# Kernel tuning notes

Hardware: AMD Instinct MI355X
Metric: run time of the kernel (lower is better)

Reference implementation:

```python
import jax, jax.numpy as jnp
import numpy as np

N_NODES = 100000  # number of graph nodes (adj is [N,N])


def setup_inputs() -> dict:
    key = jax.random.key(0)
    k1, k2, k3, k4 = jax.random.split(key, 4)
    E = 3200000
    D = 16
    row = jnp.sort(jax.random.randint(k1, (E,), 0, N_NODES, dtype=jnp.int32))
    col = jax.random.randint(k2, (E,), 0, N_NODES, dtype=jnp.int32)
    vals = jax.random.uniform(k3, (E,), dtype=jnp.float32)
    embeds = jax.random.normal(k4, (N_NODES, D), dtype=jnp.float32)
    return {"row": row, "col": col, "vals": vals, "embeds": embeds}


def reference(row, col, vals, embeds):
    # out = A @ embeds, A given in COO form: A[row[e], col[e]] = vals[e]
    # gather source features, scale by edge weight, scatter-add into rows
    msgs = vals[:, None] * embeds[col]  # [E, D]
    out = jax.ops.segment_sum(msgs, row, num_segments=N_NODES)  # [N, D]
    return out
```

## Files before the change

kernel.cpp:

```cpp
#include <hip/hip_runtime.h>
#include <hip/hip_fp16.h>


#define D 16
constexpr int BLOCK = 256;
constexpr int NPB = 64;
constexpr int SMEM_E = 3072;

typedef float f32x4 __attribute__((ext_vector_type(4)));
typedef int   i32x4 __attribute__((ext_vector_type(4)));
typedef unsigned int u32x2 __attribute__((ext_vector_type(2)));
typedef unsigned int u32x4 __attribute__((ext_vector_type(4)));

__device__ __forceinline__ unsigned cvIdx(unsigned i) { return i + ((i >> 6) << 2); }

__device__ __forceinline__ float2 h2f(unsigned u) {
  union { unsigned u; __half2 h; } c; c.u = u;
  return __half22float2(c.h);
}

__global__ __launch_bounds__(BLOCK) void prep_kernel(
    const int* __restrict__ row, int E,
    const float* __restrict__ embeds, int N,
    int* __restrict__ row_ptr, __half* __restrict__ table) {
  const long long t = (long long)blockIdx.x * BLOCK + threadIdx.x;

  if (table != nullptr) {
    if (t < (long long)N * 2) {
      const f32x4* src = (const f32x4*)embeds + t * 2;
      f32x4 a = src[0];
      f32x4 b = src[1];
      union { __half2 h[4]; u32x4 u; } o;
      o.h[0] = __floats2half2_rn(a[0], a[1]);
      o.h[1] = __floats2half2_rn(a[2], a[3]);
      o.h[2] = __floats2half2_rn(b[0], b[1]);
      o.h[3] = __floats2half2_rn(b[2], b[3]);
      *((u32x4*)table + t) = o.u;
    }
  }

  const long long e = t * 4;
  if (e < E) {
    int prev = (e == 0) ? -1 : row[e - 1];
    const int cnt = (E - e >= 4) ? 4 : (int)(E - e);
    int r[4];
    if (cnt == 4) {
      i32x4 r4 = *(const i32x4*)(row + e);
      r[0] = r4[0]; r[1] = r4[1]; r[2] = r4[2]; r[3] = r4[3];
    } else {
      for (int k = 0; k < cnt; ++k) r[k] = row[e + k];
    }
    for (int k = 0; k < cnt; ++k) {
      for (int n = prev + 1; n <= r[k]; ++n) row_ptr[n] = (int)e + k;
      prev = r[k];
    }
    if (e + cnt == E) {
      for (int n = prev + 1; n <= N; ++n) row_ptr[n] = E;
    }
  }
}

__device__ __forceinline__ void ldmeta(const unsigned* __restrict__ s_cv,
                                       unsigned i0, u32x4 M[4]) {
  const unsigned ci = cvIdx(i0 * 2);
  M[0] = *(const u32x4*)(s_cv + ci);
  M[1] = *(const u32x4*)(s_cv + ci + 4);
  M[2] = *(const u32x4*)(s_cv + ci + 8);
  M[3] = *(const u32x4*)(s_cv + ci + 12);
}

__device__ __forceinline__ void gath(const char* __restrict__ tb,
                                     const u32x4 M[4], unsigned q8, u32x2 G[8]) {
  G[0] = *(const u32x2*)(tb + (size_t)(M[0][0] << 5) + q8);
  G[1] = *(const u32x2*)(tb + (size_t)(M[0][2] << 5) + q8);
  G[2] = *(const u32x2*)(tb + (size_t)(M[1][0] << 5) + q8);
  G[3] = *(const u32x2*)(tb + (size_t)(M[1][2] << 5) + q8);
  G[4] = *(const u32x2*)(tb + (size_t)(M[2][0] << 5) + q8);
  G[5] = *(const u32x2*)(tb + (size_t)(M[2][2] << 5) + q8);
  G[6] = *(const u32x2*)(tb + (size_t)(M[3][0] << 5) + q8);
  G[7] = *(const u32x2*)(tb + (size_t)(M[3][2] << 5) + q8);
}

__device__ __forceinline__ void cons8(f32x4& acc, const u32x4 M[4],
                                      const u32x2 G[8], int e, int gb,
                                      unsigned span) {
  const unsigned vv[8] = {M[0][1], M[0][3], M[1][1], M[1][3],
                          M[2][1], M[2][3], M[3][1], M[3][3]};
  #pragma unroll
  for (int i = 0; i < 8; ++i) {
    const float w = ((unsigned)(e + i - gb) < span) ? __uint_as_float(vv[i]) : 0.f;
    const float2 lo = h2f(G[i][0]), hi = h2f(G[i][1]);
    acc[0] = fmaf(w, lo.x, acc[0]);
    acc[1] = fmaf(w, lo.y, acc[1]);
    acc[2] = fmaf(w, hi.x, acc[2]);
    acc[3] = fmaf(w, hi.y, acc[3]);
  }
}

__global__ __launch_bounds__(BLOCK) void gcn_half_kernel(
    const int* __restrict__ col, const float* __restrict__ vals,
    const __half* __restrict__ table, const int* __restrict__ row_ptr,
    f32x4* __restrict__ out4, int N, int E) {
  __shared__ __align__(16) unsigned s_cv[SMEM_E * 2 + (SMEM_E * 2 / 64) * 4];

  const int t = threadIdx.x;
  const int n0 = blockIdx.x * NPB;
  const int nEnd = (n0 + NPB < N) ? n0 + NPB : N;
  const int g = t >> 2;
  const unsigned q8 = (unsigned)((t & 3) << 3);
  const int node = n0 + g;
  const bool active = (node < nEnd);

  const int Wb = row_ptr[n0] & ~3;
  const int We = row_ptr[nEnd];
  const int beg = active ? row_ptr[node] : 0;
  const int end = active ? row_ptr[node + 1] : 0;
  const char* tb = (const char*)table;

  f32x4 acc = {0.f, 0.f, 0.f, 0.f};

  for (int W0 = Wb; W0 < We; W0 += SMEM_E) {
    const int cnt  = (SMEM_E < We - W0) ? SMEM_E : (We - W0);
    const int cntP = (cnt + 7) & ~7;
    __syncthreads();
    for (int i = t * 4; i < cntP; i += BLOCK * 4) {
      const int e = W0 + i;
      unsigned c[4], v[4];
      if (e + 3 < E) {
        i32x4 c4 = *(const i32x4*)(col + e);
        f32x4 v4 = *(const f32x4*)(vals + e);
        #pragma unroll
        for (int k = 0; k < 4; ++k) {
          c[k] = (unsigned)c4[k];
          v[k] = __float_as_uint(v4[k]);
        }
      } else {
        #pragma unroll
        for (int k = 0; k < 4; ++k) {
          const bool ok = (e + k < E);
          c[k] = ok ? (unsigned)col[e + k] : 0u;
          v[k] = ok ? __float_as_uint(vals[e + k]) : 0u;
        }
      }
      *(u32x4*)(s_cv + cvIdx((unsigned)i * 2))     = (u32x4){c[0], v[0], c[1], v[1]};
      *(u32x4*)(s_cv + cvIdx((unsigned)i * 2) + 4) = (u32x4){c[2], v[2], c[3], v[3]};
    }
    __syncthreads();

    const int gb = (beg > W0) ? beg : W0;
    const int ge = (end < W0 + cnt) ? end : (W0 + cnt);
    if (ge > gb) {
      const unsigned span = (unsigned)(ge - gb);
      const int e0 = W0 + ((gb - W0) & ~7);
      const int e1 = e0 + ((ge - e0 + 7) & ~7);
      const int eL = e1 - 8;

      u32x4 M0[4], M1[4], M2[4];
      u32x2 G0[8], G1[8];
      const int p1 = (e0 + 8 < eL) ? e0 + 8 : eL;
      ldmeta(s_cv, (unsigned)(e0 - W0), M0);
      ldmeta(s_cv, (unsigned)(p1 - W0), M1);
      gath(tb, M0, q8, G0);

      for (int e = e0; e < e1; e += 8) {
        const int p2 = (e + 16 < eL) ? e + 16 : eL;
        ldmeta(s_cv, (unsigned)(p2 - W0), M2);
        gath(tb, M1, q8, G1);
        __builtin_amdgcn_sched_barrier(0);
        cons8(acc, M0, G0, e, gb, span);
        #pragma unroll
        for (int j = 0; j < 4; ++j) { M0[j] = M1[j]; M1[j] = M2[j]; }
        #pragma unroll
        for (int j = 0; j < 8; ++j) { G0[j] = G1[j]; }
      }
    }
  }

  if (active) {
    __builtin_nontemporal_store(acc, out4 + (size_t)node * 4 + (t & 3));
  }
}

__global__ __launch_bounds__(BLOCK) void gcn_node_f32_kernel(
    const int* __restrict__ col, const float* __restrict__ vals,
    const f32x4* __restrict__ embeds4, const int* __restrict__ row_ptr,
    f32x4* __restrict__ out4, int N, int E) {
  const int t = blockIdx.x * BLOCK + threadIdx.x;
  const int node = t >> 2;
  const int q = t & 3;
  if (node >= N) return;
  const int beg = row_ptr[node];
  const int end = row_ptr[node + 1];
  f32x4 acc = {0.f, 0.f, 0.f, 0.f};
  for (int e = beg; e < end; ++e) {
    acc += vals[e] * embeds4[(long long)col[e] * 4 + q];
  }
  __builtin_nontemporal_store(acc, out4 + (long long)node * 4 + q);
}

extern "C" void kernel_launch(void* const* d_in, const int* in_sizes, int n_in,
                              void* d_out, int out_size, void* d_ws, size_t ws_size,
                              hipStream_t stream) {
  const int*   row    = (const int*)d_in[0];
  const int*   col    = (const int*)d_in[1];
  const float* vals   = (const float*)d_in[2];
  const float* embeds = (const float*)d_in[3];

  const int E = in_sizes[0];
  const int N = in_sizes[3] / D;

  const size_t rp_bytes  = ((size_t)(N + 1) * 4 + 511) & ~(size_t)511;
  const size_t tbl_bytes = (size_t)N * D * sizeof(__half);
  const bool use_half = (ws_size >= rp_bytes + tbl_bytes) && (E >= 8);

  int*    row_ptr = (int*)d_ws;
  __half* table   = use_half ? (__half*)((char*)d_ws + rp_bytes) : nullptr;

  {
    long long chunksB = ((long long)E + 3) / 4;
    long long chunksA = use_half ? (long long)N * 2 : 0;
    long long threads = chunksB > chunksA ? chunksB : chunksA;
    int grid = (int)((threads + BLOCK - 1) / BLOCK);
    prep_kernel<<<grid, BLOCK, 0, stream>>>(row, E, embeds, N, row_ptr, table);
  }
  if (use_half) {
    const int grid = (N + NPB - 1) / NPB;
    gcn_half_kernel<<<grid, BLOCK, 0, stream>>>(
        col, vals, table, row_ptr, (f32x4*)d_out, N, E);
  } else {
    long long threads = (long long)N * 4;
    int grid = (int)((threads + BLOCK - 1) / BLOCK);
    gcn_node_f32_kernel<<<grid, BLOCK, 0, stream>>>(
        col, vals, (const f32x4*)embeds, row_ptr, (f32x4*)d_out, N, E);
  }
}
```

Before: 40.58 us.

## Split edges across lane pairs with 16-byte gathers and shuffle reduction

```diff
diff --git a/kernel.cpp b/kernel.cpp
--- a/kernel.cpp
+++ b/kernel.cpp
@@ -9,7 +9,6 @@
 
 typedef float f32x4 __attribute__((ext_vector_type(4)));
 typedef int   i32x4 __attribute__((ext_vector_type(4)));
-typedef unsigned int u32x2 __attribute__((ext_vector_type(2)));
 typedef unsigned int u32x4 __attribute__((ext_vector_type(4)));
 
 __device__ __forceinline__ unsigned cvIdx(unsigned i) { return i + ((i >> 6) << 2); }
@@ -60,54 +59,19 @@
   }
 }
 
-__device__ __forceinline__ void ldmeta(const unsigned* __restrict__ s_cv,
-                                       unsigned i0, u32x4 M[4]) {
-  const unsigned ci = cvIdx(i0 * 2);
-  M[0] = *(const u32x4*)(s_cv + ci);
-  M[1] = *(const u32x4*)(s_cv + ci + 4);
-  M[2] = *(const u32x4*)(s_cv + ci + 8);
-  M[3] = *(const u32x4*)(s_cv + ci + 12);
-}
-
-__device__ __forceinline__ void gath(const char* __restrict__ tb,
-                                     const u32x4 M[4], unsigned q8, u32x2 G[8]) {
-  G[0] = *(const u32x2*)(tb + (size_t)(M[0][0] << 5) + q8);
-  G[1] = *(const u32x2*)(tb + (size_t)(M[0][2] << 5) + q8);
-  G[2] = *(const u32x2*)(tb + (size_t)(M[1][0] << 5) + q8);
-  G[3] = *(const u32x2*)(tb + (size_t)(M[1][2] << 5) + q8);
-  G[4] = *(const u32x2*)(tb + (size_t)(M[2][0] << 5) + q8);
-  G[5] = *(const u32x2*)(tb + (size_t)(M[2][2] << 5) + q8);
-  G[6] = *(const u32x2*)(tb + (size_t)(M[3][0] << 5) + q8);
-  G[7] = *(const u32x2*)(tb + (size_t)(M[3][2] << 5) + q8);
-}
-
-__device__ __forceinline__ void cons8(f32x4& acc, const u32x4 M[4],
-                                      const u32x2 G[8], int e, int gb,
-                                      unsigned span) {
-  const unsigned vv[8] = {M[0][1], M[0][3], M[1][1], M[1][3],
-                          M[2][1], M[2][3], M[3][1], M[3][3]};
-  #pragma unroll
-  for (int i = 0; i < 8; ++i) {
-    const float w = ((unsigned)(e + i - gb) < span) ? __uint_as_float(vv[i]) : 0.f;
-    const float2 lo = h2f(G[i][0]), hi = h2f(G[i][1]);
-    acc[0] = fmaf(w, lo.x, acc[0]);
-    acc[1] = fmaf(w, lo.y, acc[1]);
-    acc[2] = fmaf(w, hi.x, acc[2]);
-    acc[3] = fmaf(w, hi.y, acc[3]);
-  }
-}
-
 __global__ __launch_bounds__(BLOCK) void gcn_half_kernel(
     const int* __restrict__ col, const float* __restrict__ vals,
     const __half* __restrict__ table, const int* __restrict__ row_ptr,
-    f32x4* __restrict__ out4, int N, int E) {
+    float* __restrict__ out, int N, int E) {
   __shared__ __align__(16) unsigned s_cv[SMEM_E * 2 + (SMEM_E * 2 / 64) * 4];
 
   const int t = threadIdx.x;
   const int n0 = blockIdx.x * NPB;
   const int nEnd = (n0 + NPB < N) ? n0 + NPB : N;
   const int g = t >> 2;
-  const unsigned q8 = (unsigned)((t & 3) << 3);
+  const unsigned l = (unsigned)(t & 3);
+  const unsigned s = l >> 1;
+  const unsigned h16 = (l & 1) << 4;
   const int node = n0 + g;
   const bool active = (node < nEnd);
 
@@ -117,7 +81,7 @@
   const int end = active ? row_ptr[node + 1] : 0;
   const char* tb = (const char*)table;
 
-  f32x4 acc = {0.f, 0.f, 0.f, 0.f};
+  float acc[8] = {0.f, 0.f, 0.f, 0.f, 0.f, 0.f, 0.f, 0.f};
 
   for (int W0 = Wb; W0 < We; W0 += SMEM_E) {
     const int cnt  = (SMEM_E < We - W0) ? SMEM_E : (We - W0);
@@ -153,31 +117,54 @@
       const unsigned span = (unsigned)(ge - gb);
       const int e0 = W0 + ((gb - W0) & ~7);
       const int e1 = e0 + ((ge - e0 + 7) & ~7);
-      const int eL = e1 - 8;
-
-      u32x4 M0[4], M1[4], M2[4];
-      u32x2 G0[8], G1[8];
-      const int p1 = (e0 + 8 < eL) ? e0 + 8 : eL;
-      ldmeta(s_cv, (unsigned)(e0 - W0), M0);
-      ldmeta(s_cv, (unsigned)(p1 - W0), M1);
-      gath(tb, M0, q8, G0);
 
       for (int e = e0; e < e1; e += 8) {
-        const int p2 = (e + 16 < eL) ? e + 16 : eL;
-        ldmeta(s_cv, (unsigned)(p2 - W0), M2);
-        gath(tb, M1, q8, G1);
-        __builtin_amdgcn_sched_barrier(0);
-        cons8(acc, M0, G0, e, gb, span);
-        #pragma unroll
-        for (int j = 0; j < 4; ++j) { M0[j] = M1[j]; M1[j] = M2[j]; }
-        #pragma unroll
-        for (int j = 0; j < 8; ++j) { G0[j] = G1[j]; }
+        const unsigned ci = cvIdx((unsigned)(e - W0) * 2);
+        u32x4 M0 = *(const u32x4*)(s_cv + ci);
+        u32x4 M1 = *(const u32x4*)(s_cv + ci + 4);
+        u32x4 M2 = *(const u32x4*)(s_cv + ci + 8);
+        u32x4 M3 = *(const u32x4*)(s_cv + ci + 12);
+        const unsigned c0 = M0[s << 1], w0b = M0[(s << 1) + 1];
+        const unsigned c1 = M1[s << 1], w1b = M1[(s << 1) + 1];
+        const unsigned c2 = M2[s << 1], w2b = M2[(s << 1) + 1];
+        const unsigned c3 = M3[s << 1], w3b = M3[(s << 1) + 1];
+        u32x4 G0 = *(const u32x4*)(tb + ((size_t)c0 << 5) + h16);
+        u32x4 G1 = *(const u32x4*)(tb + ((size_t)c1 << 5) + h16);
+        u32x4 G2 = *(const u32x4*)(tb + ((size_t)c2 << 5) + h16);
+        u32x4 G3 = *(const u32x4*)(tb + ((size_t)c3 << 5) + h16);
+#define EDGE(k, GG, wb)                                                     \
+        {                                                                   \
+          const float w = ((unsigned)(e + 2 * k + (int)s - gb) < span)      \
+                              ? __uint_as_float(wb) : 0.f;                  \
+          const float2 f0 = h2f(GG[0]), f1 = h2f(GG[1]);                    \
+          const float2 f2 = h2f(GG[2]), f3 = h2f(GG[3]);                    \
+          acc[0] = fmaf(w, f0.x, acc[0]);                                   \
+          acc[1] = fmaf(w, f0.y, acc[1]);                                   \
+          acc[2] = fmaf(w, f1.x, acc[2]);                                   \
+          acc[3] = fmaf(w, f1.y, acc[3]);                                   \
+          acc[4] = fmaf(w, f2.x, acc[4]);                                   \
+          acc[5] = fmaf(w, f2.y, acc[5]);                                   \
+          acc[6] = fmaf(w, f3.x, acc[6]);                                   \
+          acc[7] = fmaf(w, f3.y, acc[7]);                                   \
+        }
+        EDGE(0, G0, w0b)
+        EDGE(1, G1, w1b)
+        EDGE(2, G2, w2b)
+        EDGE(3, G3, w3b)
+#undef EDGE
       }
     }
   }
 
-  if (active) {
-    __builtin_nontemporal_store(acc, out4 + (size_t)node * 4 + (t & 3));
+  #pragma unroll
+  for (int j = 0; j < 8; ++j) acc[j] += __shfl_xor(acc[j], 2, 64);
+
+  if (active && s == 0) {
+    float* p = out + (size_t)node * D + (l & 1) * 8;
+    f32x4 lo = {acc[0], acc[1], acc[2], acc[3]};
+    f32x4 hi = {acc[4], acc[5], acc[6], acc[7]};
+    __builtin_nontemporal_store(lo, (f32x4*)p);
+    __builtin_nontemporal_store(hi, (f32x4*)(p + 4));
   }
 }
 
@@ -226,7 +213,7 @@
   if (use_half) {
     const int grid = (N + NPB - 1) / NPB;
     gcn_half_kernel<<<grid, BLOCK, 0, stream>>>(
-        col, vals, table, row_ptr, (f32x4*)d_out, N, E);
+        col, vals, table, row_ptr, (float*)d_out, N, E);
   } else {
     long long threads = (long long)N * 4;
     int grid = (int)((threads + BLOCK - 1) / BLOCK);
```

Result: faster. 38.20 us (-5.9%).
